# Kernel optimization log

Measured on AMD Instinct MI355X. Metric: run time of the kernel, lower is better.

Reference implementation:

```python
import jax, jax.numpy as jnp
import numpy as np

# MalConv-style dims: byte vocab, tiny embed, wide stride-=kernel gated conv
B, T, V, E, C, K, S, N = 8, 1048576, 257, 8, 128, 512, 512, 64


def setup_inputs() -> dict:
    key = jax.random.key(0)
    k1, k2, k3, k4 = jax.random.split(key, 4)
    x = jax.random.randint(k1, (B, T), 0, V, dtype=jnp.int32)
    emb = jax.random.normal(k2, (V, E), dtype=jnp.float32) * 0.02
    fan = 1.0 / np.sqrt(E * K)
    w1 = jax.random.normal(k3, (C, E, K), dtype=jnp.float32) * fan
    w2 = jax.random.normal(k4, (C, E, K), dtype=jnp.float32) * fan
    b1 = jnp.zeros((C,), jnp.float32)
    b2 = jnp.zeros((C,), jnp.float32)
    return {"x": x, "emb": emb, "w1": w1, "b1": b1, "w2": w2, "b2": b2}


def reference(x, emb, w1, b1, w2, b2):
    # preprocess: byte embedding -> (B, E, T)
    z = emb[x].transpose(0, 2, 1)
    dn = ("NCH", "OIH", "NCH")
    # GatedConvolution: c1 * sigmoid(c2), valid conv, stride S -> (B, C, L)
    c1 = jax.lax.conv_general_dilated(z, w1, (S,), "VALID", dimension_numbers=dn) + b1[None, :, None]
    c2 = jax.lax.conv_general_dilated(z, w2, (S,), "VALID", dimension_numbers=dn) + b2[None, :, None]
    g = c1 * jax.nn.sigmoid(c2)  # (B, C, L)
    L = g.shape[-1]
    # input-space position of each conv output window; patch assignment
    pos = jnp.arange(L, dtype=jnp.int32) * S
    patch_size = -(-T // N)  # ceil(T / num_patches)
    seg = jnp.clip(pos // patch_size, 0, N - 1)  # (L,)
    # per-patch max-over-time, per channel: segment_max over the L axis
    gl = g.transpose(2, 0, 1).reshape(L, B * C)  # (L, B*C)
    mv = jax.ops.segment_max(gl, seg, num_segments=N)  # (N, B*C)
    max_vals = mv.reshape(N, B, C).transpose(1, 0, 2)  # (B, N, C)
    return max_vals
```

## Files before the change

### kernel.cpp

```cpp
#include <hip/hip_runtime.h>
#include <hip/hip_bf16.h>
#include <math.h>


typedef __bf16 bf16x8 __attribute__((ext_vector_type(8)));
typedef float  f32x4  __attribute__((ext_vector_type(4)));

#define WS_WP_OFF   0
#define WS_EMB_OFF  (2u << 20)

__device__ __forceinline__ void load_lds16(const void* g, void* l) {
    __builtin_amdgcn_global_load_lds(
        (const __attribute__((address_space(1))) void*)g,
        (__attribute__((address_space(3))) void*)l,
        16, 0, 0);
}

__global__ void prep_kernel(const float* __restrict__ w1,
                            const float* __restrict__ w2,
                            const float* __restrict__ emb,
                            uint4* __restrict__ Wp4,
                            __bf16* __restrict__ embp) {
    int bid = blockIdx.x;
    int tid = threadIdx.x;
    if (bid < 128) {
        __shared__ __bf16 lds[8192];
        int cb = bid & 7;
        int sB = bid >> 3;
        int nt = cb >> 1, nhalf = cb & 1;
        const float* wsrc = (nhalf ? w2 : w1) + ((size_t)(nt << 5) << 12);
        int j4  = tid & 7;
        int pr0 = tid >> 3;
#pragma unroll
        for (int p = 0; p < 8; ++p) {
            int pair = p * 32 + pr0;
            int cl = pair >> 3, e = pair & 7;
            const float4 v = *(const float4*)(wsrc + ((size_t)cl << 12) + (e << 9) + (sB << 5) + (j4 << 2));
            float vv[4] = {v.x, v.y, v.z, v.w};
#pragma unroll
            for (int jj = 0; jj < 4; ++jj) {
                int j = (j4 << 2) + jj;
                int qq = j >> 3, tt = j & 7;
                lds[(((qq << 3) + tt) * 32 + cl) * 8 + e] = (__bf16)vv[jj];
            }
        }
        __syncthreads();
        const uint4* l4 = (const uint4*)lds;
        int base = (nt << 15) + (sB << 11) + (nhalf << 5);
#pragma unroll
        for (int it = 0; it < 4; ++it) {
            int idx = it * 256 + tid;
            int qq = idx >> 8, tt = (idx >> 5) & 7, w = idx & 31;
            Wp4[base + (tt << 8) + (qq << 6) + w] = l4[idx];
        }
    } else {
        for (int i = tid; i < 2056; i += 256) embp[i] = (__bf16)emb[i];
    }
}

__global__ __launch_bounds__(256, 1)
void gemm_kernel(const int* __restrict__ x,
                 const __bf16* __restrict__ Wp,
                 const uint4* __restrict__ embp,
                 const float* __restrict__ b1,
                 const float* __restrict__ b2,
                 float* __restrict__ out) {
    __shared__ uint4 ldsB[2][2048];
    __shared__ uint4 embl[257];

    const int tid  = threadIdx.x;
    const int wave = tid >> 6;
    const int lane = tid & 63;
    const int q    = lane >> 4;
    const int nl   = lane & 15;

    for (int i = tid; i < 257; i += 256) embl[i] = embp[i];

    const int bid = blockIdx.x;
    const int mt = ((bid >> 5) << 3) | (bid & 7);
    const int nt = (bid >> 3) & 3;
    const int m0 = mt << 8;
    const int rA = m0 + (wave << 6) + nl;
    const char* WpBase = (const char*)Wp + ((size_t)nt << 19);

    const int* xp[4];
#pragma unroll
    for (int rg = 0; rg < 4; ++rg)
        xp[rg] = x + (size_t)(rA + (rg << 4)) * 512 + (q << 3);

    int4 xc[4][2];
#pragma unroll
    for (int rg = 0; rg < 4; ++rg) {
        xc[rg][0] = *(const int4*)xp[rg];
        xc[rg][1] = *(const int4*)(xp[rg] + 4);
    }
    {
        const char* src = WpBase + tid * 16;
        char* dst = (char*)&ldsB[0][0] + tid * 16;
#pragma unroll
        for (int i = 0; i < 8; ++i) load_lds16(src + i * 4096, dst + i * 4096);
    }
    __syncthreads();

    f32x4 acc[4][4] = {};

    for (int sp = 0; sp < 16; ++sp) {
        const int buf = sp & 1;
        if (sp + 1 < 16) {
            const char* src = WpBase + ((size_t)(sp + 1) << 15) + tid * 16;
            char* dst = (char*)&ldsB[buf ^ 1][0] + tid * 16;
#pragma unroll
            for (int i = 0; i < 8; ++i) load_lds16(src + i * 4096, dst + i * 4096);
        }
        int idx[4][8];
#pragma unroll
        for (int rg = 0; rg < 4; ++rg) {
            idx[rg][0] = xc[rg][0].x; idx[rg][1] = xc[rg][0].y;
            idx[rg][2] = xc[rg][0].z; idx[rg][3] = xc[rg][0].w;
            idx[rg][4] = xc[rg][1].x; idx[rg][5] = xc[rg][1].y;
            idx[rg][6] = xc[rg][1].z; idx[rg][7] = xc[rg][1].w;
        }
        const int spn = (sp + 1 < 16) ? sp + 1 : sp;
#pragma unroll
        for (int rg = 0; rg < 4; ++rg) {
            const int* p = xp[rg] + (spn << 5);
            xc[rg][0] = *(const int4*)p;
            xc[rg][1] = *(const int4*)(p + 4);
        }
        const char* Bbase = (const char*)&ldsB[buf][0] + (q << 10) + (nl << 4);
#pragma unroll
        for (int t = 0; t < 8; ++t) {
            bf16x8 a[4];
#pragma unroll
            for (int rg = 0; rg < 4; ++rg)
                a[rg] = *reinterpret_cast<const bf16x8*>(&embl[idx[rg][t]]);
#pragma unroll
            for (int nf = 0; nf < 4; ++nf) {
                bf16x8 b = *reinterpret_cast<const bf16x8*>(Bbase + (t << 12) + (nf << 8));
#pragma unroll
                for (int rg = 0; rg < 4; ++rg)
                    acc[rg][nf] = __builtin_amdgcn_mfma_f32_16x16x32_bf16(a[rg], b, acc[rg][nf], 0, 0, 0);
            }
        }
        __syncthreads();
    }

    float bb1[2], bb2[2];
#pragma unroll
    for (int nf = 0; nf < 2; ++nf) {
        int ch = (nt << 5) + (nf << 4) + nl;
        bb1[nf] = b1[ch];
        bb2[nf] = b2[ch];
    }
#pragma unroll
    for (int ph = 0; ph < 2; ++ph) {
#pragma unroll
        for (int nf = 0; nf < 2; ++nf) {
            float v = -INFINITY;
#pragma unroll
            for (int rh = 0; rh < 2; ++rh) {
                int rg = (ph << 1) + rh;
#pragma unroll
                for (int i = 0; i < 4; ++i) {
                    float c1 = acc[rg][nf][i] + bb1[nf];
                    float c2 = acc[rg][nf + 2][i] + bb2[nf];
                    float g = c1 * (1.0f / (1.0f + __expf(-c2)));
                    v = fmaxf(v, g);
                }
            }
            v = fmaxf(v, __shfl_xor(v, 16));
            v = fmaxf(v, __shfl_xor(v, 32));
            if (lane < 16) {
                int P = (mt << 3) + (wave << 1) + ph;
                out[(size_t)P * 128 + (nt << 5) + (nf << 4) + nl] = v;
            }
        }
    }
}

extern "C" void kernel_launch(void* const* d_in, const int* in_sizes, int n_in,
                              void* d_out, int out_size, void* d_ws, size_t ws_size,
                              hipStream_t stream) {
    const int*   x   = (const int*)d_in[0];
    const float* emb = (const float*)d_in[1];
    const float* w1  = (const float*)d_in[2];
    const float* b1  = (const float*)d_in[3];
    const float* w2  = (const float*)d_in[4];
    const float* b2  = (const float*)d_in[5];
    float* out = (float*)d_out;

    char* ws = (char*)d_ws;
    __bf16* Wp   = (__bf16*)(ws + WS_WP_OFF);
    __bf16* embp = (__bf16*)(ws + WS_EMB_OFF);

    prep_kernel<<<129, 256, 0, stream>>>(w1, w2, emb, (uint4*)Wp, embp);
    gemm_kernel<<<256, 256, 0, stream>>>(x, Wp, (const uint4*)embp, b1, b2, out);
}
```

Before: 125.8 us.

## Stream weight fragments from global into registers instead of LDS staging

Removes the double-buffered LDS staging of the packed weights and the per-step block barrier. Each lane now loads its weight fragments straight from global memory (L2-resident) into a two-deep register pipeline, fetching two steps ahead, and the embedding-row LDS gathers are software-pipelined one step ahead. This trades LDS traffic and barriers for more global load latency to hide and more register pressure, since every wave now fetches the weight data redundantly.

```diff
diff --git a/kernel.cpp b/kernel.cpp
--- a/kernel.cpp
+++ b/kernel.cpp
@@ -8,13 +8,6 @@
 
 #define WS_WP_OFF   0
 #define WS_EMB_OFF  (2u << 20)
-
-__device__ __forceinline__ void load_lds16(const void* g, void* l) {
-    __builtin_amdgcn_global_load_lds(
-        (const __attribute__((address_space(1))) void*)g,
-        (__attribute__((address_space(3))) void*)l,
-        16, 0, 0);
-}
 
 __global__ void prep_kernel(const float* __restrict__ w1,
                             const float* __restrict__ w2,
@@ -65,7 +58,6 @@
                  const float* __restrict__ b1,
                  const float* __restrict__ b2,
                  float* __restrict__ out) {
-    __shared__ uint4 ldsB[2][2048];
     __shared__ uint4 embl[257];
 
     const int tid  = threadIdx.x;
@@ -81,7 +73,8 @@
     const int nt = (bid >> 3) & 3;
     const int m0 = mt << 8;
     const int rA = m0 + (wave << 6) + nl;
-    const char* WpBase = (const char*)Wp + ((size_t)nt << 19);
+
+    const char* Bflat = (const char*)Wp + ((size_t)nt << 19) + (q << 10) + (nl << 4);
 
     const int* xp[4];
 #pragma unroll
@@ -94,24 +87,19 @@
         xc[rg][0] = *(const int4*)xp[rg];
         xc[rg][1] = *(const int4*)(xp[rg] + 4);
     }
-    {
-        const char* src = WpBase + tid * 16;
-        char* dst = (char*)&ldsB[0][0] + tid * 16;
-#pragma unroll
-        for (int i = 0; i < 8; ++i) load_lds16(src + i * 4096, dst + i * 4096);
-    }
+
+    bf16x8 bb[2][4];
+#pragma unroll
+    for (int nf = 0; nf < 4; ++nf) {
+        bb[0][nf] = *reinterpret_cast<const bf16x8*>(Bflat + (nf << 8));
+        bb[1][nf] = *reinterpret_cast<const bf16x8*>(Bflat + 4096 + (nf << 8));
+    }
+
     __syncthreads();
 
     f32x4 acc[4][4] = {};
 
     for (int sp = 0; sp < 16; ++sp) {
-        const int buf = sp & 1;
-        if (sp + 1 < 16) {
-            const char* src = WpBase + ((size_t)(sp + 1) << 15) + tid * 16;
-            char* dst = (char*)&ldsB[buf ^ 1][0] + tid * 16;
-#pragma unroll
-            for (int i = 0; i < 8; ++i) load_lds16(src + i * 4096, dst + i * 4096);
-        }
         int idx[4][8];
 #pragma unroll
         for (int rg = 0; rg < 4; ++rg) {
@@ -120,29 +108,43 @@
             idx[rg][4] = xc[rg][1].x; idx[rg][5] = xc[rg][1].y;
             idx[rg][6] = xc[rg][1].z; idx[rg][7] = xc[rg][1].w;
         }
-        const int spn = (sp + 1 < 16) ? sp + 1 : sp;
-#pragma unroll
-        for (int rg = 0; rg < 4; ++rg) {
-            const int* p = xp[rg] + (spn << 5);
-            xc[rg][0] = *(const int4*)p;
-            xc[rg][1] = *(const int4*)(p + 4);
-        }
-        const char* Bbase = (const char*)&ldsB[buf][0] + (q << 10) + (nl << 4);
+        if (sp < 15) {
+#pragma unroll
+            for (int rg = 0; rg < 4; ++rg) {
+                const int* p = xp[rg] + ((sp + 1) << 5);
+                xc[rg][0] = *(const int4*)p;
+                xc[rg][1] = *(const int4*)(p + 4);
+            }
+        }
+
+        bf16x8 aa[2][4];
+#pragma unroll
+        for (int rg = 0; rg < 4; ++rg)
+            aa[0][rg] = *reinterpret_cast<const bf16x8*>(&embl[idx[rg][0]]);
+
 #pragma unroll
         for (int t = 0; t < 8; ++t) {
-            bf16x8 a[4];
-#pragma unroll
-            for (int rg = 0; rg < 4; ++rg)
-                a[rg] = *reinterpret_cast<const bf16x8*>(&embl[idx[rg][t]]);
+            if (t < 7) {
+#pragma unroll
+                for (int rg = 0; rg < 4; ++rg)
+                    aa[(t + 1) & 1][rg] = *reinterpret_cast<const bf16x8*>(&embl[idx[rg][t + 1]]);
+            }
 #pragma unroll
             for (int nf = 0; nf < 4; ++nf) {
-                bf16x8 b = *reinterpret_cast<const bf16x8*>(Bbase + (t << 12) + (nf << 8));
 #pragma unroll
                 for (int rg = 0; rg < 4; ++rg)
-                    acc[rg][nf] = __builtin_amdgcn_mfma_f32_16x16x32_bf16(a[rg], b, acc[rg][nf], 0, 0, 0);
-            }
-        }
-        __syncthreads();
+                    acc[rg][nf] = __builtin_amdgcn_mfma_f32_16x16x32_bf16(
+                        aa[t & 1][rg], bb[t & 1][nf], acc[rg][nf], 0, 0, 0);
+            }
+            {
+                int gt2 = (sp << 3) + t + 2;
+                if (gt2 > 127) gt2 = 127;
+                const char* pb = Bflat + ((size_t)gt2 << 12);
+#pragma unroll
+                for (int nf = 0; nf < 4; ++nf)
+                    bb[t & 1][nf] = *reinterpret_cast<const bf16x8*>(pb + (nf << 8));
+            }
+        }
     }
 
     float bb1[2], bb2[2];
```

Result: slower. 155.5 us (+23.6%).
